# Kernel tuning notes

Measured on AMD Instinct MI355X. Metric: run time of the kernel, lower is better.

The kernel has to match this reference:

```python
import jax, jax.numpy as jnp
import numpy as np
import math

DIM = 512
HEADS = 8
DIM_HEAD = 64
INNER = HEADS * DIM_HEAD


def setup_inputs() -> dict:
    key = jax.random.key(0)
    k1, k2, k3, k4 = jax.random.split(key, 4)
    x = jax.random.normal(k1, (8, 1024, DIM), dtype=jnp.float32)
    w_qkv = jax.random.normal(k2, (DIM, INNER * 3), dtype=jnp.float32) / math.sqrt(DIM)
    w_out = jax.random.normal(k3, (INNER, DIM), dtype=jnp.float32) / math.sqrt(INNER)
    temperature = jnp.array(math.log(DIM_HEAD ** -0.5), dtype=jnp.float32)
    return {"x": x, "w_qkv": w_qkv, "w_out": w_out, "temperature": temperature}


def reference(x, w_qkv, w_out, temperature):
    b, n, _ = x.shape
    qkv = x @ w_qkv  # [b, n, 3*inner]
    q, k, v = jnp.split(qkv, 3, axis=-1)
    # [b, n, h*d] -> [b, h, n, d]
    def split_heads(t):
        return t.reshape(b, n, HEADS, DIM_HEAD).transpose(0, 2, 1, 3)
    q, k, v = split_heads(q), split_heads(k), split_heads(v)
    dots = jnp.einsum('bhnd,bhmd->bhnm', q, k) * jnp.exp(temperature)
    mask_value = -jnp.finfo(dots.dtype).max
    eye = jnp.eye(n, dtype=bool)
    dots = jnp.where(eye, mask_value, dots)
    attn = jax.nn.softmax(dots, axis=-1)
    out = jnp.einsum('bhnm,bhmd->bhnd', attn, v)
    out = out.transpose(0, 2, 1, 3).reshape(b, n, INNER)
    return out @ w_out
```

## Files before the change

### kernel.cpp

```cpp
#include <hip/hip_runtime.h>
#include <math.h>

#define BATCH  8
#define SEQ    1024
#define DMODEL 512
#define NHEADS 8
#define DHEAD  64
#define MTOT   (BATCH*SEQ)
#define QKVLD  (3*DMODEL)

typedef unsigned short ushortT;
typedef __attribute__((ext_vector_type(8))) short short8;
typedef __attribute__((ext_vector_type(4))) float f32x4;

typedef __attribute__((address_space(3))) unsigned char lds_byte;
typedef __attribute__((address_space(1))) const unsigned char glob_byte;

__device__ inline void g2l16(const void* g, void* l) {
    __builtin_amdgcn_global_load_lds((glob_byte*)g, (lds_byte*)l, 16, 0, 0);
}

__device__ inline ushortT f2bf(float f) {
    union { float f; unsigned u; } v; v.f = f;
    unsigned r = (v.u + 0x7FFFu + ((v.u >> 16) & 1u)) >> 16;
    return (ushortT)r;
}
__device__ inline ushortT f2bf_fast(float f) {
    union { float f; unsigned u; } v; v.f = f;
    return (ushortT)((v.u + 0x8000u) >> 16);
}

__global__ __launch_bounds__(256)
void cvt_bf16(const float* __restrict__ in, ushortT* __restrict__ out, int n8)
{
    int gid = blockIdx.x * 256 + threadIdx.x;
    if (gid >= n8) return;
    const float4 a = *(const float4*)(in + (long)gid*8);
    const float4 b = *(const float4*)(in + (long)gid*8 + 4);
    ushortT o[8];
    o[0]=f2bf(a.x); o[1]=f2bf(a.y); o[2]=f2bf(a.z); o[3]=f2bf(a.w);
    o[4]=f2bf(b.x); o[5]=f2bf(b.y); o[6]=f2bf(b.z); o[7]=f2bf(b.w);
    *(short8*)(out + (long)gid*8) = *(short8*)o;
}

__global__ __launch_bounds__(256)
void cvt_transpose(const float* __restrict__ W, ushortT* __restrict__ WT,
                   int K, int N)
{
    __shared__ float T[32][33];
    const int t = threadIdx.x;
    const int n0 = blockIdx.x * 32;
    const int k0 = blockIdx.y * 32;
    {
        const int r = t >> 3, c4 = (t & 7) * 4;
        const float4 v = *(const float4*)(W + (long)(k0 + r)*N + n0 + c4);
        T[c4+0][r] = v.x; T[c4+1][r] = v.y; T[c4+2][r] = v.z; T[c4+3][r] = v.w;
    }
    __syncthreads();
    {
        const int n = t >> 3, k4 = (t & 7) * 4;
        ushortT o[4];
        o[0] = f2bf(T[n][k4+0]); o[1] = f2bf(T[n][k4+1]);
        o[2] = f2bf(T[n][k4+2]); o[3] = f2bf(T[n][k4+3]);
        *(uint2*)(WT + (long)(n0 + n)*K + k0 + k4) = *(uint2*)o;
    }
}

template <int OUT_BF16>
__global__ __launch_bounds__(256, 3)
void gemm_bf16(const ushortT* __restrict__ A, const ushortT* __restrict__ BT,
               void* __restrict__ Cv, int M, int N, int K)
{
    __shared__ ushortT As[128*64];
    __shared__ ushortT Bs[128*64];

    const int t    = threadIdx.x;
    const int lane = t & 63;
    const int w    = t >> 6;
    const int l15  = lane & 15, l4 = lane >> 4;

    const int nwg = gridDim.x * gridDim.y;
    const int bid = blockIdx.y * gridDim.x + blockIdx.x;
    const int swz = (bid & 7) * (nwg >> 3) + (bid >> 3);
    const int bm  = swz / gridDim.x;
    const int bn  = swz % gridDim.x;

    const int srow = t >> 3;
    const int slot = t & 7;

    f32x4 acc[4][4] = {};

    for (int kt = 0; kt < K; kt += 64) {
#pragma unroll
        for (int c = 0; c < 4; ++c) {
            const int row  = c*32 + srow;
            const int scol = ((slot ^ (row & 7)) << 4);
            g2l16((const char*)(A  + (long)(bm*128 + row)*K + kt) + scol,
                  (char*)As + c*4096 + t*16);
            g2l16((const char*)(BT + (long)(bn*128 + row)*K + kt) + scol,
                  (char*)Bs + c*4096 + t*16);
        }
        asm volatile("s_waitcnt vmcnt(0)" ::: "memory");
        __syncthreads();

#pragma unroll
        for (int kk = 0; kk < 2; ++kk) {
            short8 a[4], b[4];
#pragma unroll
            for (int i = 0; i < 4; ++i) {
                const int ra = (w >> 1)*64 + i*16 + l15;
                const int ca = (kk*32 + l4*8) ^ ((ra & 7) << 3);
                a[i] = *(const short8*)&As[ra*64 + ca];
                const int rb = (w & 1)*64 + i*16 + l15;
                const int cb = (kk*32 + l4*8) ^ ((rb & 7) << 3);
                b[i] = *(const short8*)&Bs[rb*64 + cb];
            }
#pragma unroll
            for (int i = 0; i < 4; ++i)
#pragma unroll
                for (int j = 0; j < 4; ++j)
                    acc[i][j] = __builtin_amdgcn_mfma_f32_16x16x32_bf16(
                                    a[i], b[j], acc[i][j], 0, 0, 0);
        }
        __syncthreads();
    }

#pragma unroll
    for (int i = 0; i < 4; ++i) {
        const int row0 = bm*128 + (w >> 1)*64 + i*16 + l4*4;
#pragma unroll
        for (int j = 0; j < 4; ++j) {
            const int col = bn*128 + (w & 1)*64 + j*16 + l15;
#pragma unroll
            for (int r = 0; r < 4; ++r) {
                const float v = acc[i][j][r];
                if (OUT_BF16) ((ushortT*)Cv)[(long)(row0 + r)*N + col] = f2bf(v);
                else          ((float*)Cv)[(long)(row0 + r)*N + col]   = v;
            }
        }
    }
}

__global__ __launch_bounds__(256, 4)
void attn_mfma(const ushortT* __restrict__ qkv, ushortT* __restrict__ aout,
               const float* __restrict__ temp)
{
    __shared__ ushortT Ps[64*64];
    __shared__ ushortT Ks[2][64*64];
    __shared__ ushortT Vt[2][64*64];

    const int t    = threadIdx.x;
    const int lane = t & 63;
    const int w    = t >> 6;
    const int l15  = lane & 15, l4 = lane >> 4;
    const int bh   = blockIdx.x;
    const int qb   = blockIdx.y;
    const int b    = bh >> 3, h = bh & 7;

    const float scale2 = __expf(temp[0]) * 1.44269504f;
    const long  row0   = (long)b * SEQ * QKVLD;

    const int vkey = ((t & 3) << 4) | ((t >> 2) & 15);
    const int vd0  = w * 16;

    short8 onesf;
#pragma unroll
    for (int e = 0; e < 8; ++e) onesf[e] = (short)0x3F80;

    {
        const char* qbase = (const char*)(qkv + row0 + (long)qb*64*QKVLD + h*DHEAD);
        const char* kbase = (const char*)(qkv + row0 + DMODEL + h*DHEAD);
#pragma unroll
        for (int c = 0; c < 2; ++c) {
            const int row  = c*32 + (t >> 3);
            const int scol = ((t & 7) ^ (row & 7)) << 4;
            g2l16(qbase + (long)row*(QKVLD*2) + scol, (char*)Ps + c*4096 + t*16);
            g2l16(kbase + (long)row*(QKVLD*2) + scol, (char*)&Ks[0][0] + c*4096 + t*16);
        }
        const ushortT* vbase = qkv + row0 + 2*DMODEL + h*DHEAD;
        ushortT vv[16];
        *(short8*)&vv[0] = *(const short8*)(vbase + (long)vkey*QKVLD + vd0);
        *(short8*)&vv[8] = *(const short8*)(vbase + (long)vkey*QKVLD + vd0 + 8);
        asm volatile("s_waitcnt vmcnt(0)" ::: "memory");
#pragma unroll
        for (int e = 0; e < 16; ++e) {
            const int row = vd0 + e;
            Vt[0][row*64 + (vkey ^ ((row & 7) << 3))] = vv[e];
        }
        __syncthreads();
    }

    short8 qa[2];
#pragma unroll
    for (int kk = 0; kk < 2; ++kk) {
        const int r = w*16 + l15;
        const int c = (kk*32 + l4*8) ^ ((r & 7) << 3);
        qa[kk] = *(const short8*)&Ps[r*64 + c];
    }

    f32x4 o_[4] = {};
    f32x4 lacc  = {};

    for (int jt = 0; jt < 16; ++jt) {
        const int cur = jt & 1, nxt = cur ^ 1;
        const bool pf = (jt + 1) < 16;

        ushortT vv[16];
        if (pf) {
            const char* kbase = (const char*)(qkv + row0 + (long)(jt+1)*64*QKVLD
                                              + DMODEL + h*DHEAD);
#pragma unroll
            for (int c = 0; c < 2; ++c) {
                const int row  = c*32 + (t >> 3);
                const int scol = ((t & 7) ^ (row & 7)) << 4;
                g2l16(kbase + (long)row*(QKVLD*2) + scol,
                      (char*)&Ks[nxt][0] + c*4096 + t*16);
            }
            const ushortT* vbase = qkv + row0 + (long)(jt+1)*64*QKVLD
                                   + 2*DMODEL + h*DHEAD;
            *(short8*)&vv[0] = *(const short8*)(vbase + (long)vkey*QKVLD + vd0);
            *(short8*)&vv[8] = *(const short8*)(vbase + (long)vkey*QKVLD + vd0 + 8);
        }

        f32x4 s_[4] = {};
#pragma unroll
        for (int kk = 0; kk < 2; ++kk) {
            short8 kb[4];
#pragma unroll
            for (int j = 0; j < 4; ++j) {
                const int r = j*16 + l15;
                const int c = (kk*32 + l4*8) ^ ((r & 7) << 3);
                kb[j] = *(const short8*)&Ks[cur][r*64 + c];
            }
#pragma unroll
            for (int j = 0; j < 4; ++j)
                s_[j] = __builtin_amdgcn_mfma_f32_16x16x32_bf16(
                            qa[kk], kb[j], s_[j], 0, 0, 0);
        }

#pragma unroll
        for (int r = 0; r < 4; ++r) {
            const int lrow = w*16 + l4*4 + r;
            const int grow = qb*64 + lrow;
#pragma unroll
            for (int j = 0; j < 4; ++j) {
                const int gcol = jt*64 + j*16 + l15;
                float x = s_[j][r] * scale2;
                x = (gcol == grow) ? -1e30f : x;
                const float p = exp2f(x);
                Ps[lrow*64 + ((j*16 + l15) ^ ((lrow & 7) << 3))] = f2bf_fast(p);
            }
        }

#pragma unroll
        for (int kk = 0; kk < 2; ++kk) {
            const int rp = w*16 + l15;
            const int cp = (kk*32 + l4*8) ^ ((rp & 7) << 3);
            const short8 pa = *(const short8*)&Ps[rp*64 + cp];
            lacc = __builtin_amdgcn_mfma_f32_16x16x32_bf16(pa, onesf, lacc, 0, 0, 0);
            short8 vb[4];
#pragma unroll
            for (int j = 0; j < 4; ++j) {
                const int r = j*16 + l15;
                const int c = (kk*32 + l4*8) ^ ((r & 7) << 3);
                vb[j] = *(const short8*)&Vt[cur][r*64 + c];
            }
#pragma unroll
            for (int j = 0; j < 4; ++j)
                o_[j] = __builtin_amdgcn_mfma_f32_16x16x32_bf16(
                            pa, vb[j], o_[j], 0, 0, 0);
        }

        if (pf) {
            asm volatile("s_waitcnt vmcnt(0)" ::: "memory");
#pragma unroll
            for (int e = 0; e < 16; ++e) {
                const int row = vd0 + e;
                Vt[nxt][row*64 + (vkey ^ ((row & 7) << 3))] = vv[e];
            }
        }
        __syncthreads();
    }

#pragma unroll
    for (int r = 0; r < 4; ++r) {
        const float inv  = 1.0f / lacc[r];
        const long  grow = (long)b*SEQ + qb*64 + w*16 + l4*4 + r;
#pragma unroll
        for (int j = 0; j < 4; ++j)
            aout[grow*DMODEL + h*DHEAD + j*16 + l15] = f2bf(o_[j][r] * inv);
    }
}

extern "C" void kernel_launch(void* const* d_in, const int* in_sizes, int n_in,
                              void* d_out, int out_size, void* d_ws, size_t ws_size,
                              hipStream_t stream)
{
    const float* x     = (const float*)d_in[0];
    const float* w_qkv = (const float*)d_in[1];
    const float* w_out = (const float*)d_in[2];
    const float* temp  = (const float*)d_in[3];
    float* out = (float*)d_out;

    char* ws = (char*)d_ws;
    ushortT* x_bf   = (ushortT*)(ws);
    ushortT* wqkvT  = (ushortT*)(ws + 8388608);
    ushortT* woutT  = (ushortT*)(ws + 9961472);
    ushortT* qkv_bf = (ushortT*)(ws + 10485760);
    ushortT* aout   = (ushortT*)(ws + 35651584);

    cvt_bf16<<<dim3((MTOT*DMODEL/8)/256), 256, 0, stream>>>(x, x_bf, MTOT*DMODEL/8);
    cvt_transpose<<<dim3(QKVLD/32, DMODEL/32), 256, 0, stream>>>(w_qkv, wqkvT, DMODEL, QKVLD);
    cvt_transpose<<<dim3(DMODEL/32, DMODEL/32), 256, 0, stream>>>(w_out, woutT, DMODEL, DMODEL);

    gemm_bf16<1><<<dim3(QKVLD/128, MTOT/128), 256, 0, stream>>>(
        x_bf, wqkvT, qkv_bf, MTOT, QKVLD, DMODEL);

    attn_mfma<<<dim3(BATCH*NHEADS, SEQ/64), 256, 0, stream>>>(qkv_bf, aout, temp);

    gemm_bf16<0><<<dim3(DMODEL/128, MTOT/128), 256, 0, stream>>>(
        aout, woutT, out, MTOT, DMODEL, DMODEL);
}
```

Baseline: 152.6 us.

## Emit transposed V and pre-scaled Q from QKV GEMM epilogue for attention

```diff
diff --git a/kernel.cpp b/kernel.cpp
--- a/kernel.cpp
+++ b/kernel.cpp
@@ -66,10 +66,11 @@
     }
 }
 
-template <int OUT_BF16>
+template <int MODE>
 __global__ __launch_bounds__(256, 3)
 void gemm_bf16(const ushortT* __restrict__ A, const ushortT* __restrict__ BT,
-               void* __restrict__ Cv, int M, int N, int K)
+               void* __restrict__ Cv, ushortT* __restrict__ vT,
+               const float* __restrict__ temp, int M, int N, int K)
 {
     __shared__ ushortT As[128*64];
     __shared__ ushortT Bs[128*64];
@@ -125,6 +126,27 @@
         __syncthreads();
     }
 
+    if (MODE == 1 && bn >= 8) {
+#pragma unroll
+        for (int i = 0; i < 4; ++i) {
+            const int row0 = bm*128 + (w >> 1)*64 + i*16 + l4*4;
+            const int bb   = row0 >> 10, n = row0 & 1023;
+#pragma unroll
+            for (int j = 0; j < 4; ++j) {
+                const int cg = bn*128 + (w & 1)*64 + j*16 + l15 - 1024;
+                const int h = cg >> 6, d = cg & 63;
+                union { ushortT u[4]; uint2 q; } pk;
+#pragma unroll
+                for (int r = 0; r < 4; ++r) pk.u[r] = f2bf(acc[i][j][r]);
+                *(uint2*)&vT[((long)((bb*8 + h)*64 + d))*1024 + n] = pk.q;
+            }
+        }
+        return;
+    }
+
+    const float qs = (MODE == 1) ? __expf(temp[0]) * 1.44269504f : 1.0f;
+    const float mulv = (MODE == 1 && bn < 4) ? qs : 1.0f;
+
 #pragma unroll
     for (int i = 0; i < 4; ++i) {
         const int row0 = bm*128 + (w >> 1)*64 + i*16 + l4*4;
@@ -133,21 +155,21 @@
             const int col = bn*128 + (w & 1)*64 + j*16 + l15;
 #pragma unroll
             for (int r = 0; r < 4; ++r) {
-                const float v = acc[i][j][r];
-                if (OUT_BF16) ((ushortT*)Cv)[(long)(row0 + r)*N + col] = f2bf(v);
-                else          ((float*)Cv)[(long)(row0 + r)*N + col]   = v;
+                const float v = acc[i][j][r] * mulv;
+                if (MODE == 1) ((ushortT*)Cv)[(long)(row0 + r)*N + col] = f2bf(v);
+                else           ((float*)Cv)[(long)(row0 + r)*N + col]   = v;
             }
         }
     }
 }
 
 __global__ __launch_bounds__(256, 4)
-void attn_mfma(const ushortT* __restrict__ qkv, ushortT* __restrict__ aout,
-               const float* __restrict__ temp)
+void attn_mfma(const ushortT* __restrict__ qkv, const ushortT* __restrict__ vT,
+               ushortT* __restrict__ aout)
 {
     __shared__ ushortT Ps[64*64];
     __shared__ ushortT Ks[2][64*64];
-    __shared__ ushortT Vt[2][64*64];
+    __shared__ ushortT Vs[2][64*64];
 
     const int t    = threadIdx.x;
     const int lane = t & 63;
@@ -157,11 +179,8 @@
     const int qb   = blockIdx.y;
     const int b    = bh >> 3, h = bh & 7;
 
-    const float scale2 = __expf(temp[0]) * 1.44269504f;
-    const long  row0   = (long)b * SEQ * QKVLD;
-
-    const int vkey = ((t & 3) << 4) | ((t >> 2) & 15);
-    const int vd0  = w * 16;
+    const long row0 = (long)b * SEQ * QKVLD;
+    const char* vtb = (const char*)(vT + (long)bh * 64 * 1024);
 
     short8 onesf;
 #pragma unroll
@@ -176,17 +195,9 @@
             const int scol = ((t & 7) ^ (row & 7)) << 4;
             g2l16(qbase + (long)row*(QKVLD*2) + scol, (char*)Ps + c*4096 + t*16);
             g2l16(kbase + (long)row*(QKVLD*2) + scol, (char*)&Ks[0][0] + c*4096 + t*16);
-        }
-        const ushortT* vbase = qkv + row0 + 2*DMODEL + h*DHEAD;
-        ushortT vv[16];
-        *(short8*)&vv[0] = *(const short8*)(vbase + (long)vkey*QKVLD + vd0);
-        *(short8*)&vv[8] = *(const short8*)(vbase + (long)vkey*QKVLD + vd0 + 8);
+            g2l16(vtb + (long)row*2048 + scol,        (char*)&Vs[0][0] + c*4096 + t*16);
+        }
         asm volatile("s_waitcnt vmcnt(0)" ::: "memory");
-#pragma unroll
-        for (int e = 0; e < 16; ++e) {
-            const int row = vd0 + e;
-            Vt[0][row*64 + (vkey ^ ((row & 7) << 3))] = vv[e];
-        }
         __syncthreads();
     }
 
@@ -205,7 +216,6 @@
         const int cur = jt & 1, nxt = cur ^ 1;
         const bool pf = (jt + 1) < 16;
 
-        ushortT vv[16];
         if (pf) {
             const char* kbase = (const char*)(qkv + row0 + (long)(jt+1)*64*QKVLD
                                               + DMODEL + h*DHEAD);
@@ -215,11 +225,9 @@
                 const int scol = ((t & 7) ^ (row & 7)) << 4;
                 g2l16(kbase + (long)row*(QKVLD*2) + scol,
                       (char*)&Ks[nxt][0] + c*4096 + t*16);
-            }
-            const ushortT* vbase = qkv + row0 + (long)(jt+1)*64*QKVLD
-                                   + 2*DMODEL + h*DHEAD;
-            *(short8*)&vv[0] = *(const short8*)(vbase + (long)vkey*QKVLD + vd0);
-            *(short8*)&vv[8] = *(const short8*)(vbase + (long)vkey*QKVLD + vd0 + 8);
+                g2l16(vtb + (long)row*2048 + (jt+1)*128 + scol,
+                      (char*)&Vs[nxt][0] + c*4096 + t*16);
+            }
         }
 
         f32x4 s_[4] = {};
@@ -238,17 +246,26 @@
                             qa[kk], kb[j], s_[j], 0, 0, 0);
         }
 
-#pragma unroll
-        for (int r = 0; r < 4; ++r) {
-            const int lrow = w*16 + l4*4 + r;
-            const int grow = qb*64 + lrow;
-#pragma unroll
-            for (int j = 0; j < 4; ++j) {
-                const int gcol = jt*64 + j*16 + l15;
-                float x = s_[j][r] * scale2;
-                x = (gcol == grow) ? -1e30f : x;
-                const float p = exp2f(x);
-                Ps[lrow*64 + ((j*16 + l15) ^ ((lrow & 7) << 3))] = f2bf_fast(p);
+        if (jt == qb) {
+#pragma unroll
+            for (int r = 0; r < 4; ++r) {
+                const int lrow = w*16 + l4*4 + r;
+#pragma unroll
+                for (int j = 0; j < 4; ++j) {
+                    float p = exp2f(s_[j][r]);
+                    if (j*16 + l15 == lrow) p = 0.f;
+                    Ps[lrow*64 + ((j*16 + l15) ^ ((lrow & 7) << 3))] = f2bf_fast(p);
+                }
+            }
+        } else {
+#pragma unroll
+            for (int r = 0; r < 4; ++r) {
+                const int lrow = w*16 + l4*4 + r;
+#pragma unroll
+                for (int j = 0; j < 4; ++j) {
+                    const float p = exp2f(s_[j][r]);
+                    Ps[lrow*64 + ((j*16 + l15) ^ ((lrow & 7) << 3))] = f2bf_fast(p);
+                }
             }
         }
 
@@ -263,7 +280,7 @@
             for (int j = 0; j < 4; ++j) {
                 const int r = j*16 + l15;
                 const int c = (kk*32 + l4*8) ^ ((r & 7) << 3);
-                vb[j] = *(const short8*)&Vt[cur][r*64 + c];
+                vb[j] = *(const short8*)&Vs[cur][r*64 + c];
             }
 #pragma unroll
             for (int j = 0; j < 4; ++j)
@@ -271,14 +288,7 @@
                             pa, vb[j], o_[j], 0, 0, 0);
         }
 
-        if (pf) {
-            asm volatile("s_waitcnt vmcnt(0)" ::: "memory");
-#pragma unroll
-            for (int e = 0; e < 16; ++e) {
-                const int row = vd0 + e;
-                Vt[nxt][row*64 + (vkey ^ ((row & 7) << 3))] = vv[e];
-            }
-        }
+        if (pf) asm volatile("s_waitcnt vmcnt(0)" ::: "memory");
         __syncthreads();
     }
 
@@ -307,17 +317,18 @@
     ushortT* wqkvT  = (ushortT*)(ws + 8388608);
     ushortT* woutT  = (ushortT*)(ws + 9961472);
     ushortT* qkv_bf = (ushortT*)(ws + 10485760);
-    ushortT* aout   = (ushortT*)(ws + 35651584);
+    ushortT* vT     = (ushortT*)(ws + 35651584);
+    ushortT* aout   = (ushortT*)(ws + 44040192);
 
     cvt_bf16<<<dim3((MTOT*DMODEL/8)/256), 256, 0, stream>>>(x, x_bf, MTOT*DMODEL/8);
     cvt_transpose<<<dim3(QKVLD/32, DMODEL/32), 256, 0, stream>>>(w_qkv, wqkvT, DMODEL, QKVLD);
     cvt_transpose<<<dim3(DMODEL/32, DMODEL/32), 256, 0, stream>>>(w_out, woutT, DMODEL, DMODEL);
 
     gemm_bf16<1><<<dim3(QKVLD/128, MTOT/128), 256, 0, stream>>>(
-        x_bf, wqkvT, qkv_bf, MTOT, QKVLD, DMODEL);
-
-    attn_mfma<<<dim3(BATCH*NHEADS, SEQ/64), 256, 0, stream>>>(qkv_bf, aout, temp);
+        x_bf, wqkvT, qkv_bf, vT, temp, MTOT, QKVLD, DMODEL);
+
+    attn_mfma<<<dim3(BATCH*NHEADS, SEQ/64), 256, 0, stream>>>(qkv_bf, vT, aout);
 
     gemm_bf16<0><<<dim3(DMODEL/128, MTOT/128), 256, 0, stream>>>(
-        aout, woutT, out, MTOT, DMODEL, DMODEL);
-}
+        aout, woutT, out, nullptr, nullptr, MTOT, DMODEL, DMODEL);
+}
```

New measurement: 146.0 us. 1.04x faster.
